# Kernel tuning notes

Measured on AMD Instinct MI355X. Metric: run time of the kernel, lower is better.

The kernel has to match this reference:

```python
import jax, jax.numpy as jnp
import numpy as np
from jax import lax

EPS = 1e-5
CLIP = 1.3  # Hardtanh(-1.3, 1.3)


def hardtanh(v):
    return jnp.clip(v, -CLIP, CLIP)


def binarize(v):
    # sign() forward with straight-through (identity) gradient, as in BCNN BinarizeF
    return v + lax.stop_gradient(jnp.sign(v) - v)


def bc_conv(x, w):
    # binarized conv: binarize both activations and weights, 3x3, stride 1, pad 1
    return lax.conv_general_dilated(
        binarize(x), binarize(w),
        window_strides=(1, 1), padding=((1, 1), (1, 1)),
        dimension_numbers=("NCHW", "OIHW", "NCHW"))


def batchnorm(v, gamma, beta):
    # batch statistics over (N, H, W), per-channel affine (DC_Bn4 variant)
    mean = jnp.mean(v, axis=(0, 2, 3), keepdims=True)
    var = jnp.var(v, axis=(0, 2, 3), keepdims=True)
    inv = lax.rsqrt(var + EPS)
    return (v - mean) * inv * gamma[None, :, None, None] + beta[None, :, None, None]


def setup_inputs() -> dict:
    key = jax.random.key(0)
    k_x, k_w1, k_w2 = jax.random.split(key, 3)
    C = 32
    x = jax.random.normal(k_x, (16, C, 224, 224), dtype=jnp.float32)
    w1 = jax.random.normal(k_w1, (C, C, 3, 3), dtype=jnp.float32) * 0.1
    w2 = jax.random.normal(k_w2, (C, C, 3, 3), dtype=jnp.float32) * 0.1
    g1 = jnp.ones((C,), jnp.float32); b1 = jnp.zeros((C,), jnp.float32)
    g2 = jnp.ones((C,), jnp.float32); b2 = jnp.zeros((C,), jnp.float32)
    return {"x": x, "w1": w1, "g1": g1, "b1": b1, "w2": w2, "g2": g2, "b2": b2}


def reference(x, w1, g1, b1, w2, g2, b2):
    y = batchnorm(bc_conv(hardtanh(x), w1), g1, b1)
    y = batchnorm(bc_conv(hardtanh(y), w2), g2, b2)
    return x + y
```

## Files before the change

kernel.cpp:

```cpp
#include <hip/hip_runtime.h>
#include <stdint.h>

#define NB 16
#define CC 32
#define HH 224
#define WW 224
#define HWP (HH*WW)
#define NHWP (NB*HWP)
#define PW 226
#define PSZ (PW*PW)

#define OFF_S1   0u
#define OFF_S2   3268864u
#define OFF_WP1  6537728u
#define OFF_WP2  6538880u
#define OFF_SQ1  6540032u
#define OFF_SQ2  6544128u
#define OFF_SUM1 6548224u
#define OFF_SUM2 6550272u
#define OFF_BF1  6552320u
#define OFF_BF2  6561536u

typedef int v4i    __attribute__((ext_vector_type(4)));
typedef int i32x16 __attribute__((ext_vector_type(16)));

__global__ void __launch_bounds__(256) k_setup(const uint32_t* __restrict__ w1,
                                               const uint32_t* __restrict__ w2,
                                               char* __restrict__ ws) {
    int t = blockIdx.x * 256 + threadIdx.x;
    if (t < 576) {
        const uint32_t* w = (t < 288) ? w1 : w2;
        uint32_t* o = (uint32_t*)(ws + ((t < 288) ? OFF_WP1 : OFF_WP2));
        int idx = (t < 288) ? t : t - 288;
        int oc = idx / 9, k = idx - oc * 9;
        uint32_t word = 0;
        for (int i = 0; i < 32; ++i)
            word |= (w[(oc * 32 + i) * 9 + k] >> 31) << i;
        o[idx] = word;
    } else if (t < 3648) {
        ((uint32_t*)(ws + OFF_SQ1))[t - 576] = 0u;
    } else if (t >= 4096 && t < 32896) {
        int b = t - 4096;
        uint32_t* buf = (uint32_t*)(ws + ((b < 14400) ? OFF_S1 : OFF_S2));
        int bb = (b < 14400) ? b : b - 14400;
        int n = bb / 900;
        int e = bb - n * 900;
        int row, col;
        if (e < 226)      { row = 0;   col = e; }
        else if (e < 452) { row = 225; col = e - 226; }
        else { int k = e - 452; row = 1 + (k >> 1); col = (k & 1) ? 225 : 0; }
        buf[(size_t)n * PSZ + row * PW + col] = 0u;
    } else if (t >= 32896 && t < 34048) {
        int idx = t - 32896;
        int layer = idx / 576, rem = idx - layer * 576;
        int tap = rem / 64, lane = rem - tap * 64;
        int oc = lane & 31, kb = (lane >> 5) * 16;
        const uint32_t* w = layer ? w2 : w1;
        uint32_t dw[4];
        #pragma unroll
        for (int d = 0; d < 4; ++d) {
            uint32_t v = 0x01010101u;
            #pragma unroll
            for (int b = 0; b < 4; ++b) {
                uint32_t sgn = w[(oc * 32 + kb + 4 * d + b) * 9 + tap] >> 31;
                v ^= (0xFEu * sgn) << (8 * b);
            }
            dw[d] = v;
        }
        uint4* o = (uint4*)(ws + (layer ? OFF_BF2 : OFF_BF1));
        o[tap * 64 + lane] = make_uint4(dw[0], dw[1], dw[2], dw[3]);
    }
}

__global__ void __launch_bounds__(256) k_packx(const uint32_t* __restrict__ x,
                                               uint32_t* __restrict__ sp) {
    int t = blockIdx.x * 256 + threadIdx.x;
    int n = t / (HWP / 4);
    int rem4 = t - n * (HWP / 4);
    int px0 = rem4 * 4;
    int r = px0 / WW;
    int cw0 = px0 - r * WW;
    const uint32_t* xp = x + (size_t)n * CC * HWP + px0;
    uint32_t w0 = 0, w1 = 0, w2 = 0, w3 = 0;
    #pragma unroll
    for (int c = 0; c < 32; ++c) {
        uint4 v = *reinterpret_cast<const uint4*>(xp + (size_t)c * HWP);
        w0 |= (v.x >> 31) << c;
        w1 |= (v.y >> 31) << c;
        w2 |= (v.z >> 31) << c;
        w3 |= (v.w >> 31) << c;
    }
    uint32_t* op = sp + (size_t)n * PSZ + (r + 1) * PW + (cw0 + 1);
    op[0] = w0; op[1] = w1; op[2] = w2; op[3] = w3;
}

#define ASTRIDE 48
#define AROW (226*ASTRIDE)

__device__ __forceinline__ uint32_t spread4(uint32_t nib) {
    uint32_t s = (nib & 1u) | ((nib & 2u) << 7) | ((nib & 4u) << 14) | ((nib & 8u) << 21);
    return 0x01010101u ^ (s * 0xFEu);
}

__device__ __forceinline__ i32x16 conv_mfma(const uint32_t* __restrict__ sp,
                                            const v4i* __restrict__ bfp,
                                            int n, int r, char* At) {
    for (int s = threadIdx.x; s < 3 * 226; s += 448) {
        int dr = s / 226, cc = s - dr * 226;
        int srow = r - 1 + dr, scol = cc - 1;
        uint32_t d8[8];
        if (srow < 0 || srow >= HH || scol < 0 || scol >= WW) {
            #pragma unroll
            for (int i = 0; i < 8; ++i) d8[i] = 0u;
        } else {
            uint32_t w = sp[(size_t)n * PSZ + (srow + 1) * PW + (scol + 1)];
            #pragma unroll
            for (int i = 0; i < 8; ++i) d8[i] = spread4((w >> (4 * i)) & 0xFu);
        }
        uint32_t* p = (uint32_t*)(At + s * ASTRIDE);
        *(uint4*)(p)     = make_uint4(d8[0], d8[1], d8[2], d8[3]);
        *(uint4*)(p + 4) = make_uint4(d8[4], d8[5], d8[6], d8[7]);
    }

    int l = threadIdx.x & 63;
    v4i bf[9];
    #pragma unroll
    for (int t = 0; t < 9; ++t) bf[t] = bfp[t * 64 + l];
    __syncthreads();

    int wavebase = (threadIdx.x >> 6) * 32;
    int base = (wavebase + (l & 31)) * ASTRIDE + (l >> 5) * 16;

    i32x16 acc = {0,0,0,0,0,0,0,0,0,0,0,0,0,0,0,0};
    #pragma unroll
    for (int dh = 0; dh < 3; ++dh) {
        #pragma unroll
        for (int dw = 0; dw < 3; ++dw) {
            v4i a = *reinterpret_cast<const v4i*>(At + base + dh * AROW + dw * ASTRIDE);
            acc = __builtin_amdgcn_mfma_i32_32x32x32_i8(a, bf[dh * 3 + dw], acc, 0, 0, 0);
        }
    }
    return acc;
}

__global__ void __launch_bounds__(448) k_stats(const uint32_t* __restrict__ sp,
                                               const v4i* __restrict__ bfp,
                                               int* __restrict__ g_sum,
                                               unsigned long long* __restrict__ g_sq) {
    __shared__ __align__(16) char At[3 * 226 * ASTRIDE];
    __shared__ int ls[7][32], lq[7][32];

    int n = blockIdx.x / HH, r = blockIdx.x - n * HH;
    i32x16 acc = conv_mfma(sp, bfp, n, r, At);

    int l = threadIdx.x & 63;
    int s = 0, q = 0;
    #pragma unroll
    for (int g = 0; g < 16; ++g) { int c = acc[g]; s += c; q += c * c; }
    s += __shfl_xor(s, 32, 64);
    q += __shfl_xor(q, 32, 64);
    int wid = threadIdx.x >> 6;
    if (l < 32) { ls[wid][l] = s; lq[wid][l] = q; }
    __syncthreads();
    if (threadIdx.x < 32) {
        int S = 0, Q = 0;
        #pragma unroll
        for (int w = 0; w < 7; ++w) { S += ls[w][threadIdx.x]; Q += lq[w][threadIdx.x]; }
        int bin = blockIdx.x & 15;
        atomicAdd(&g_sum[bin * 32 + threadIdx.x], S);
        atomicAdd(&g_sq[bin * 32 + threadIdx.x], (unsigned long long)(long long)Q);
    }
}

__device__ __forceinline__ void build_affine16(const int* __restrict__ g_sum,
                                               const unsigned long long* __restrict__ g_sq,
                                               const float* __restrict__ gamma,
                                               const float* __restrict__ beta,
                                               float* aL, float* dL) {
    if (threadIdx.x < 32) {
        int c = threadIdx.x;
        int Si = 0; unsigned long long Qu = 0;
        #pragma unroll
        for (int b = 0; b < 16; ++b) { Si += g_sum[b * 32 + c]; Qu += g_sq[b * 32 + c]; }
        double M = (double)NHWP;
        double mean = (double)Si / M;
        double ex2 = (double)(long long)Qu / M;
        double var = ex2 - mean * mean;
        double inv = 1.0 / sqrt(var + 1e-5);
        double aa = inv * (double)gamma[c];
        aL[c] = (float)aa;
        dL[c] = (float)((double)beta[c] - aa * mean);
    }
}

__global__ void __launch_bounds__(448) k_sign(const uint32_t* __restrict__ sp,
                                              const v4i* __restrict__ bfp,
                                              const int* __restrict__ g_sum,
                                              const unsigned long long* __restrict__ g_sq,
                                              const float* __restrict__ gamma,
                                              const float* __restrict__ beta,
                                              uint32_t* __restrict__ op) {
    __shared__ __align__(16) char At[3 * 226 * ASTRIDE];
    __shared__ float aL[32], dL[32];
    build_affine16(g_sum, g_sq, gamma, beta, aL, dL);

    int n = blockIdx.x / HH, r = blockIdx.x - n * HH;
    i32x16 acc = conv_mfma(sp, bfp, n, r, At);

    int l = threadIdx.x & 63;
    int wavebase = (threadIdx.x >> 6) * 32;
    float a = aL[l & 31], d = dL[l & 31];
    uint32_t* orow = op + (size_t)n * PSZ + (r + 1) * PW + 1 + wavebase;
    #pragma unroll
    for (int g = 0; g < 16; ++g) {
        float y = fmaf(a, (float)acc[g], d);
        unsigned long long b = __ballot((__float_as_uint(y) >> 31) != 0u);
        if (l == 0) {
            int pxr = (g & 3) + 8 * (g >> 2);
            orow[pxr]     = (uint32_t)b;
            orow[pxr + 4] = (uint32_t)(b >> 32);
        }
    }
}

__global__ void __launch_bounds__(448) k_res(const uint32_t* __restrict__ sp,
                                             const v4i* __restrict__ bfp,
                                             const int* __restrict__ g_sum,
                                             const unsigned long long* __restrict__ g_sq,
                                             const float* __restrict__ gamma,
                                             const float* __restrict__ beta,
                                             const float* __restrict__ x,
                                             float* __restrict__ out) {
    __shared__ __align__(16) char At[3 * 226 * ASTRIDE];
    __shared__ float aL[32], dL[32];
    build_affine16(g_sum, g_sq, gamma, beta, aL, dL);

    int n = blockIdx.x / HH, r = blockIdx.x - n * HH;
    i32x16 acc = conv_mfma(sp, bfp, n, r, At);

    int l = threadIdx.x & 63;
    int oc = l & 31, hi = l >> 5;
    int wavebase = (threadIdx.x >> 6) * 32;
    float a = aL[oc], d = dL[oc];
    size_t rowoff = (size_t)n * CC * HWP + (size_t)oc * HWP + (size_t)r * WW;
    #pragma unroll
    for (int g = 0; g < 4; ++g) {
        int px0 = wavebase + 8 * g + 4 * hi;
        float4 xv = *reinterpret_cast<const float4*>(x + rowoff + px0);
        float4 ov;
        ov.x = xv.x + fmaf(a, (float)acc[4 * g + 0], d);
        ov.y = xv.y + fmaf(a, (float)acc[4 * g + 1], d);
        ov.z = xv.z + fmaf(a, (float)acc[4 * g + 2], d);
        ov.w = xv.w + fmaf(a, (float)acc[4 * g + 3], d);
        *reinterpret_cast<float4*>(out + rowoff + px0) = ov;
    }
}

extern "C" void kernel_launch(void* const* d_in, const int* in_sizes, int n_in,
                              void* d_out, int out_size, void* d_ws, size_t ws_size,
                              hipStream_t stream) {
    const float* x  = (const float*)d_in[0];
    const float* w1 = (const float*)d_in[1];
    const float* g1 = (const float*)d_in[2];
    const float* b1 = (const float*)d_in[3];
    const float* w2 = (const float*)d_in[4];
    const float* g2 = (const float*)d_in[5];
    const float* b2 = (const float*)d_in[6];
    float* out = (float*)d_out;

    char* ws = (char*)d_ws;
    uint32_t* s1  = (uint32_t*)(ws + OFF_S1);
    uint32_t* s2  = (uint32_t*)(ws + OFF_S2);
    const v4i* bf1 = (const v4i*)(ws + OFF_BF1);
    const v4i* bf2 = (const v4i*)(ws + OFF_BF2);
    unsigned long long* sq1 = (unsigned long long*)(ws + OFF_SQ1);
    unsigned long long* sq2 = (unsigned long long*)(ws + OFF_SQ2);
    int* sum1 = (int*)(ws + OFF_SUM1);
    int* sum2 = (int*)(ws + OFF_SUM2);

    k_setup<<<134, 256, 0, stream>>>((const uint32_t*)w1, (const uint32_t*)w2, ws);
    k_packx<<<784, 256, 0, stream>>>((const uint32_t*)x, s1);
    k_stats<<<3584, 448, 0, stream>>>(s1, bf1, sum1, sq1);
    k_sign <<<3584, 448, 0, stream>>>(s1, bf1, sum1, sq1, g1, b1, s2);
    k_stats<<<3584, 448, 0, stream>>>(s2, bf2, sum2, sq2);
    k_res  <<<3584, 448, 0, stream>>>(s2, bf2, sum2, sq2, g2, b2, x, out);
}
```

Baseline: 276.4 us.

## Cache int16 conv outputs in stats pass instead of recomputing convolution

The stats kernel now also writes each binary-conv result as int16 into a workspace buffer when the workspace is large enough. New elementwise kernels, k_signc and k_resc, read that buffer to apply the batchnorm affine and the sign or residual step, so the second MFMA convolution pass per layer disappears. The cost is about 51 MB of extra global writes and reads per layer. The old recompute path stays as a fallback when the workspace is too small.

```diff
diff --git a/kernel.cpp b/kernel.cpp
--- a/kernel.cpp
+++ b/kernel.cpp
@@ -20,6 +20,8 @@
 #define OFF_SUM2 6550272u
 #define OFF_BF1  6552320u
 #define OFF_BF2  6561536u
+#define OFF_CACHE 6572032u
+#define CACHE_BYTES 51380224u
 
 typedef int v4i    __attribute__((ext_vector_type(4)));
 typedef int i32x16 __attribute__((ext_vector_type(16)));
@@ -146,7 +148,8 @@
 __global__ void __launch_bounds__(448) k_stats(const uint32_t* __restrict__ sp,
                                                const v4i* __restrict__ bfp,
                                                int* __restrict__ g_sum,
-                                               unsigned long long* __restrict__ g_sq) {
+                                               unsigned long long* __restrict__ g_sq,
+                                               int16_t* __restrict__ cache) {
     __shared__ __align__(16) char At[3 * 226 * ASTRIDE];
     __shared__ int ls[7][32], lq[7][32];
 
@@ -154,6 +157,22 @@
     i32x16 acc = conv_mfma(sp, bfp, n, r, At);
 
     int l = threadIdx.x & 63;
+    if (cache) {
+        int oc = l & 31, hi = l >> 5;
+        int wavebase = (threadIdx.x >> 6) * 32;
+        int16_t* cp = cache + ((size_t)n * CC + oc) * HWP + (size_t)r * WW;
+        #pragma unroll
+        for (int g = 0; g < 4; ++g) {
+            int px0 = wavebase + 8 * g + 4 * hi;
+            short4 sv;
+            sv.x = (short)acc[4 * g + 0];
+            sv.y = (short)acc[4 * g + 1];
+            sv.z = (short)acc[4 * g + 2];
+            sv.w = (short)acc[4 * g + 3];
+            *reinterpret_cast<short4*>(cp + px0) = sv;
+        }
+    }
+
     int s = 0, q = 0;
     #pragma unroll
     for (int g = 0; g < 16; ++g) { int c = acc[g]; s += c; q += c * c; }
@@ -193,13 +212,76 @@
     }
 }
 
-__global__ void __launch_bounds__(448) k_sign(const uint32_t* __restrict__ sp,
-                                              const v4i* __restrict__ bfp,
+__global__ void __launch_bounds__(256) k_signc(const int16_t* __restrict__ cache,
+                                               const int* __restrict__ g_sum,
+                                               const unsigned long long* __restrict__ g_sq,
+                                               const float* __restrict__ gamma,
+                                               const float* __restrict__ beta,
+                                               uint32_t* __restrict__ op) {
+    __shared__ float aL[32], dL[32];
+    build_affine16(g_sum, g_sq, gamma, beta, aL, dL);
+    __syncthreads();
+
+    int t = blockIdx.x * 256 + threadIdx.x;
+    int n = t / (HWP / 4);
+    int rem4 = t - n * (HWP / 4);
+    int px0 = rem4 * 4;
+    int r = px0 / WW;
+    int cw0 = px0 - r * WW;
+    const int16_t* cp = cache + (size_t)n * CC * HWP + px0;
+    uint32_t w0 = 0, w1 = 0, w2 = 0, w3 = 0;
+    #pragma unroll
+    for (int c = 0; c < 32; ++c) {
+        short4 v = *reinterpret_cast<const short4*>(cp + (size_t)c * HWP);
+        float a = aL[c], d = dL[c];
+        w0 |= (__float_as_uint(fmaf(a, (float)v.x, d)) >> 31) << c;
+        w1 |= (__float_as_uint(fmaf(a, (float)v.y, d)) >> 31) << c;
+        w2 |= (__float_as_uint(fmaf(a, (float)v.z, d)) >> 31) << c;
+        w3 |= (__float_as_uint(fmaf(a, (float)v.w, d)) >> 31) << c;
+    }
+    uint32_t* o = op + (size_t)n * PSZ + (r + 1) * PW + (cw0 + 1);
+    o[0] = w0; o[1] = w1; o[2] = w2; o[3] = w3;
+}
+
+__global__ void __launch_bounds__(256) k_resc(const int16_t* __restrict__ cache,
                                               const int* __restrict__ g_sum,
                                               const unsigned long long* __restrict__ g_sq,
                                               const float* __restrict__ gamma,
                                               const float* __restrict__ beta,
-                                              uint32_t* __restrict__ op) {
+                                              const float* __restrict__ x,
+                                              float* __restrict__ out) {
+    __shared__ float aL[32], dL[32];
+    build_affine16(g_sum, g_sq, gamma, beta, aL, dL);
+    __syncthreads();
+
+    int t = blockIdx.x * 256 + threadIdx.x;
+    int n = t / (HWP / 4);
+    int rem4 = t - n * (HWP / 4);
+    int px0 = rem4 * 4;
+    const int16_t* cp = cache + (size_t)n * CC * HWP + px0;
+    const float* xp = x + (size_t)n * CC * HWP + px0;
+    float* op = out + (size_t)n * CC * HWP + px0;
+    #pragma unroll
+    for (int c = 0; c < 32; ++c) {
+        short4 v = *reinterpret_cast<const short4*>(cp + (size_t)c * HWP);
+        float a = aL[c], d = dL[c];
+        float4 xv = *reinterpret_cast<const float4*>(xp + (size_t)c * HWP);
+        float4 ov;
+        ov.x = xv.x + fmaf(a, (float)v.x, d);
+        ov.y = xv.y + fmaf(a, (float)v.y, d);
+        ov.z = xv.z + fmaf(a, (float)v.z, d);
+        ov.w = xv.w + fmaf(a, (float)v.w, d);
+        *reinterpret_cast<float4*>(op + (size_t)c * HWP) = ov;
+    }
+}
+
+__global__ void __launch_bounds__(448) k_sign_f(const uint32_t* __restrict__ sp,
+                                                const v4i* __restrict__ bfp,
+                                                const int* __restrict__ g_sum,
+                                                const unsigned long long* __restrict__ g_sq,
+                                                const float* __restrict__ gamma,
+                                                const float* __restrict__ beta,
+                                                uint32_t* __restrict__ op) {
     __shared__ __align__(16) char At[3 * 226 * ASTRIDE];
     __shared__ float aL[32], dL[32];
     build_affine16(g_sum, g_sq, gamma, beta, aL, dL);
@@ -223,14 +305,14 @@
     }
 }
 
-__global__ void __launch_bounds__(448) k_res(const uint32_t* __restrict__ sp,
-                                             const v4i* __restrict__ bfp,
-                                             const int* __restrict__ g_sum,
-                                             const unsigned long long* __restrict__ g_sq,
-                                             const float* __restrict__ gamma,
-                                             const float* __restrict__ beta,
-                                             const float* __restrict__ x,
-                                             float* __restrict__ out) {
+__global__ void __launch_bounds__(448) k_res_f(const uint32_t* __restrict__ sp,
+                                               const v4i* __restrict__ bfp,
+                                               const int* __restrict__ g_sum,
+                                               const unsigned long long* __restrict__ g_sq,
+                                               const float* __restrict__ gamma,
+                                               const float* __restrict__ beta,
+                                               const float* __restrict__ x,
+                                               float* __restrict__ out) {
     __shared__ __align__(16) char At[3 * 226 * ASTRIDE];
     __shared__ float aL[32], dL[32];
     build_affine16(g_sum, g_sq, gamma, beta, aL, dL);
@@ -277,11 +359,19 @@
     unsigned long long* sq2 = (unsigned long long*)(ws + OFF_SQ2);
     int* sum1 = (int*)(ws + OFF_SUM1);
     int* sum2 = (int*)(ws + OFF_SUM2);
+    bool useCache = ws_size >= (size_t)OFF_CACHE + (size_t)CACHE_BYTES;
+    int16_t* cache = useCache ? (int16_t*)(ws + OFF_CACHE) : (int16_t*)nullptr;
 
     k_setup<<<134, 256, 0, stream>>>((const uint32_t*)w1, (const uint32_t*)w2, ws);
     k_packx<<<784, 256, 0, stream>>>((const uint32_t*)x, s1);
-    k_stats<<<3584, 448, 0, stream>>>(s1, bf1, sum1, sq1);
-    k_sign <<<3584, 448, 0, stream>>>(s1, bf1, sum1, sq1, g1, b1, s2);
-    k_stats<<<3584, 448, 0, stream>>>(s2, bf2, sum2, sq2);
-    k_res  <<<3584, 448, 0, stream>>>(s2, bf2, sum2, sq2, g2, b2, x, out);
-}
+    k_stats<<<3584, 448, 0, stream>>>(s1, bf1, sum1, sq1, cache);
+    if (useCache) {
+        k_signc<<<784, 256, 0, stream>>>(cache, sum1, sq1, g1, b1, s2);
+        k_stats<<<3584, 448, 0, stream>>>(s2, bf2, sum2, sq2, cache);
+        k_resc <<<784, 256, 0, stream>>>(cache, sum2, sq2, g2, b2, x, out);
+    } else {
+        k_sign_f<<<3584, 448, 0, stream>>>(s1, bf1, sum1, sq1, g1, b1, s2);
+        k_stats<<<3584, 448, 0, stream>>>(s2, bf2, sum2, sq2, cache);
+        k_res_f<<<3584, 448, 0, stream>>>(s2, bf2, sum2, sq2, g2, b2, x, out);
+    }
+}
```

New measurement: 291.2 us. 5.4% more time.
